# Kernel tuning notes

Measured on AMD Instinct MI355X. Metric: run time of the kernel, lower is better.

## Reference

```python
import jax, jax.numpy as jnp
import numpy as np

NEG_SLOPE = 0.2  # LeakyReLU slope from the module


def setup_inputs() -> dict:
    key = jax.random.key(0)
    k1, k2, k3, k4, k5 = jax.random.split(key, 5)
    B, N, H = 8, 1024, 512
    node_features = jax.random.normal(k1, (B, N, H), dtype=jnp.float32)
    adjacency_matrix = jax.random.randint(k2, (B, N, N), 0, 2, dtype=jnp.int32)
    # attn_linear: Linear(2H, 1). Split weight into src/dst halves (same math as
    # applying it to concat([x_i, x_j])): score_ij = x_i.a_src + x_j.a_dst + b.
    scale = 1.0 / np.sqrt(2 * H)
    attn_w_src = jax.random.uniform(k3, (H,), jnp.float32, -scale, scale)
    attn_w_dst = jax.random.uniform(k4, (H,), jnp.float32, -scale, scale)
    attn_b = jax.random.uniform(k5, (1,), jnp.float32, -scale, scale)
    return {"node_features": node_features, "adjacency_matrix": adjacency_matrix,
            "attn_w_src": attn_w_src, "attn_w_dst": attn_w_dst, "attn_b": attn_b}


def reference(node_features, adjacency_matrix, attn_w_src, attn_w_dst, attn_b):
    B, N, H = node_features.shape
    # Decomposed additive scores: [B,N,1] + [B,1,N] + b  -> [B,N,N]
    s_src = jnp.einsum('bnh,h->bn', node_features, attn_w_src)
    s_dst = jnp.einsum('bnh,h->bn', node_features, attn_w_dst)
    scores = s_src[:, :, None] + s_dst[:, None, :] + attn_b[0]
    scores = jax.nn.leaky_relu(scores, negative_slope=NEG_SLOPE)
    # adjacency + self loops; mask where zero
    adj = adjacency_matrix.astype(jnp.float32) + jnp.eye(N, dtype=jnp.float32)[None]
    scores = jnp.where(adj == 0, -jnp.inf, scores)
    attn = jax.nn.softmax(scores, axis=-1)
    # dropout is identity in eval mode
    return jnp.einsum('bij,bjh->bih', attn, node_features)
```

## Files before the change

### kernel.cpp

```cpp
#include <hip/hip_runtime.h>
#include <hip/hip_bf16.h>

#define BB 8
#define NN 1024
#define HH 512
#define NEG 0.2f

typedef float f32x4 __attribute__((ext_vector_type(4)));
typedef short bf16x8 __attribute__((ext_vector_type(8)));
typedef unsigned int u32;

__device__ __forceinline__ unsigned short f2bf(float f) {
    union { float f; u32 u; } a; a.f = f;
    u32 u = a.u;
    u += 0x7fffu + ((u >> 16) & 1u);
    return (unsigned short)(u >> 16);
}

__device__ __forceinline__ void gload16(const void* g, void* l) {
    __builtin_amdgcn_global_load_lds(
        (const __attribute__((address_space(1))) unsigned int*)g,
        (__attribute__((address_space(3))) unsigned int*)l, 16, 0, 0);
}

__global__ __launch_bounds__(512) void prep_kernel(
    const float* __restrict__ x, const float* __restrict__ wsrc,
    const float* __restrict__ wdst, float* __restrict__ ssrc,
    float* __restrict__ sdst, unsigned short* __restrict__ xt)
{
    __shared__ __align__(16) unsigned short lt[16][528];

    int bid = blockIdx.x;
    int b = bid & 7;
    int j0 = (bid >> 3) * 16;
    int t = threadIdx.x;
    int r = t >> 5;
    int l = t & 31;

    const float* xrow = x + ((size_t)(b * NN + j0 + r)) * HH;
    float psrc = 0.f, pdst = 0.f;
    #pragma unroll
    for (int q = 0; q < 4; ++q) {
        int h = q * 128 + l * 4;
        f32x4 v = *(const f32x4*)(xrow + h);
        f32x4 a = *(const f32x4*)(wsrc + h);
        f32x4 d = *(const f32x4*)(wdst + h);
        psrc += v[0]*a[0] + v[1]*a[1] + v[2]*a[2] + v[3]*a[3];
        pdst += v[0]*d[0] + v[1]*d[1] + v[2]*d[2] + v[3]*d[3];
        u32 lo = (u32)f2bf(v[0]) | ((u32)f2bf(v[1]) << 16);
        u32 hi = (u32)f2bf(v[2]) | ((u32)f2bf(v[3]) << 16);
        *(u32*)&lt[r][h + 0] = lo;
        *(u32*)&lt[r][h + 2] = hi;
    }
    #pragma unroll
    for (int k = 1; k < 32; k <<= 1) {
        psrc += __shfl_xor(psrc, k);
        pdst += __shfl_xor(pdst, k);
    }
    if (l == 0) {
        ssrc[b * NN + j0 + r] = psrc;
        sdst[b * NN + j0 + r] = pdst;
    }
    __syncthreads();

    unsigned short v[16];
    #pragma unroll
    for (int rr = 0; rr < 16; ++rr) v[rr] = lt[rr][t];
    unsigned short* dst = xt + ((size_t)(b * HH + t)) * NN + j0;
    #pragma unroll
    for (int q = 0; q < 2; ++q) {
        bf16x8 pk;
        #pragma unroll
        for (int e = 0; e < 8; ++e) pk[e] = (short)v[q*8 + e];
        *(bf16x8*)(dst + q * 8) = pk;
    }
}

__global__ __launch_bounds__(256) void softmax_kernel(
    const float* __restrict__ ssrc, const float* __restrict__ sdst,
    const int* __restrict__ adj, const float* __restrict__ bptr,
    unsigned short* __restrict__ P)
{
    __shared__ __align__(16) float sd[NN];

    int bid = blockIdx.x;
    int b = bid & 7;
    int r0 = (bid >> 3) * 4;
    int t = threadIdx.x;
    int lane = t & 63;
    int w = t >> 6;

    *(f32x4*)&sd[t * 4] = *(const f32x4*)&sdst[b * NN + t * 4];
    __syncthreads();

    int ig = r0 + w;
    float si = ssrc[b * NN + ig] + bptr[0];
    const int* arow = adj + ((size_t)b * NN + ig) * NN;

    float sc[16];
    float m = -1e30f;
    #pragma unroll
    for (int it = 0; it < 4; ++it) {
        int j = it * 256 + lane * 4;
        int4 a4 = *(const int4*)(arow + j);
        f32x4 sv = *(const f32x4*)&sd[j];
        float s0 = si + sv[0]; s0 = s0 > 0.f ? s0 : NEG * s0;
        float s1 = si + sv[1]; s1 = s1 > 0.f ? s1 : NEG * s1;
        float s2 = si + sv[2]; s2 = s2 > 0.f ? s2 : NEG * s2;
        float s3 = si + sv[3]; s3 = s3 > 0.f ? s3 : NEG * s3;
        sc[it*4+0] = (a4.x != 0 || (j + 0) == ig) ? s0 : -1e30f;
        sc[it*4+1] = (a4.y != 0 || (j + 1) == ig) ? s1 : -1e30f;
        sc[it*4+2] = (a4.z != 0 || (j + 2) == ig) ? s2 : -1e30f;
        sc[it*4+3] = (a4.w != 0 || (j + 3) == ig) ? s3 : -1e30f;
        m = fmaxf(m, fmaxf(fmaxf(sc[it*4+0], sc[it*4+1]), fmaxf(sc[it*4+2], sc[it*4+3])));
    }
    #pragma unroll
    for (int k = 1; k < 64; k <<= 1) m = fmaxf(m, __shfl_xor(m, k));
    float sum = 0.f;
    #pragma unroll
    for (int k = 0; k < 16; ++k) { float e = __expf(sc[k] - m); sc[k] = e; sum += e; }
    #pragma unroll
    for (int k = 1; k < 64; k <<= 1) sum += __shfl_xor(sum, k);
    float inv = 1.f / sum;

    unsigned short* prow = P + ((size_t)b * NN + ig) * NN;
    #pragma unroll
    for (int it = 0; it < 4; ++it) {
        int j = it * 256 + lane * 4;
        u32 lo = (u32)f2bf(sc[it*4+0] * inv) | ((u32)f2bf(sc[it*4+1] * inv) << 16);
        u32 hi = (u32)f2bf(sc[it*4+2] * inv) | ((u32)f2bf(sc[it*4+3] * inv) << 16);
        *(uint2*)(prow + j) = make_uint2(lo, hi);
    }
}

__global__ __launch_bounds__(512) void pv_kernel(
    const unsigned short* __restrict__ P, const unsigned short* __restrict__ xt,
    float* __restrict__ out)
{
    __shared__ __align__(16) unsigned short As[3 * 128 * 64];
    __shared__ __align__(16) unsigned short Bs[3 * 64 * 64];

    int bid = blockIdx.x;
    int b = bid & 7;
    int tt = bid >> 3;
    int h0 = (tt & 3) * 128;
    int i0 = (tt >> 2) * 64;
    int t = threadIdx.x;
    int lane = t & 63;
    int w = t >> 6;
    int wm = w & 3;
    int wn = w >> 2;
    int g = lane >> 4;
    int ln = lane & 15;

    int row0 = t >> 3;
    int c = t & 7;
    int sj = (c ^ (row0 & 7)) * 8;
    const unsigned short* gA0 = xt + ((size_t)(b * HH + h0 + row0)) * NN + sj;
    const unsigned short* gA1 = gA0 + (size_t)64 * NN;
    const unsigned short* gB0 = P + ((size_t)(b * NN + i0 + row0)) * NN + sj;
    unsigned short* lA0 = As + t * 8;
    unsigned short* lA1 = As + 4096 + t * 8;
    unsigned short* lB0 = Bs + t * 8;

    const char* pa[2][2];
    #pragma unroll
    for (int ma = 0; ma < 2; ++ma) {
        int row = wm * 32 + ma * 16 + ln;
        #pragma unroll
        for (int kk = 0; kk < 2; ++kk)
            pa[ma][kk] = (const char*)As + ((row * 128 + kk * 64 + g * 16) ^ ((row & 7) << 4));
    }
    const char* pb[2][2];
    #pragma unroll
    for (int nb = 0; nb < 2; ++nb) {
        int row = wn * 32 + nb * 16 + ln;
        #pragma unroll
        for (int kk = 0; kk < 2; ++kk)
            pb[nb][kk] = (const char*)Bs + ((row * 128 + kk * 64 + g * 16) ^ ((row & 7) << 4));
    }

    f32x4 acc[2][2];
    #pragma unroll
    for (int ma = 0; ma < 2; ++ma)
        #pragma unroll
        for (int nb = 0; nb < 2; ++nb)
            acc[ma][nb] = (f32x4){0.f, 0.f, 0.f, 0.f};

    auto stage = [&](int p, int js) {
        int joff = js * 64;
        gload16(gA0 + joff, lA0 + p * 8192);
        gload16(gA1 + joff, lA1 + p * 8192);
        gload16(gB0 + joff, lB0 + p * 4096);
    };
    auto compute = [&](int ofsA, int ofsB) {
        bf16x8 af[2][2], bfr[2][2];
        #pragma unroll
        for (int ma = 0; ma < 2; ++ma)
            #pragma unroll
            for (int kk = 0; kk < 2; ++kk)
                af[ma][kk] = *(const bf16x8*)(pa[ma][kk] + ofsA);
        #pragma unroll
        for (int nb = 0; nb < 2; ++nb)
            #pragma unroll
            for (int kk = 0; kk < 2; ++kk)
                bfr[nb][kk] = *(const bf16x8*)(pb[nb][kk] + ofsB);
        #pragma unroll
        for (int kk = 0; kk < 2; ++kk)
            #pragma unroll
            for (int ma = 0; ma < 2; ++ma)
                #pragma unroll
                for (int nb = 0; nb < 2; ++nb)
                    acc[ma][nb] = __builtin_amdgcn_mfma_f32_16x16x32_bf16(af[ma][kk], bfr[nb][kk], acc[ma][nb], 0, 0, 0);
    };

    stage(0, 0);
    stage(1, 1);
    int cur = 0, nx2 = 2;
    for (int js = 0; js < 16; ++js) {
        if (js < 15) asm volatile("s_waitcnt vmcnt(3)" ::: "memory");
        else         asm volatile("s_waitcnt vmcnt(0)" ::: "memory");
        __builtin_amdgcn_sched_barrier(0);
        __builtin_amdgcn_s_barrier();
        if (js + 2 < 16) stage(nx2, js + 2);
        compute(cur * 16384, cur * 8192);
        cur = (cur == 2) ? 0 : cur + 1;
        nx2 = (nx2 == 2) ? 0 : nx2 + 1;
    }

    #pragma unroll
    for (int nb = 0; nb < 2; ++nb) {
        int i = i0 + wn * 32 + nb * 16 + ln;
        #pragma unroll
        for (int ma = 0; ma < 2; ++ma) {
            float* dst = out + ((size_t)(b * NN + i)) * HH + h0 + wm * 32 + ma * 16 + g * 4;
            *(f32x4*)dst = acc[ma][nb];
        }
    }
}

extern "C" void kernel_launch(void* const* d_in, const int* in_sizes, int n_in,
                              void* d_out, int out_size, void* d_ws, size_t ws_size,
                              hipStream_t stream) {
    const float* x    = (const float*)d_in[0];
    const int*   adj  = (const int*)d_in[1];
    const float* wsrc = (const float*)d_in[2];
    const float* wdst = (const float*)d_in[3];
    const float* bias = (const float*)d_in[4];
    float* out = (float*)d_out;

    float* ssrc = (float*)d_ws;
    float* sdst = ssrc + BB * NN;
    unsigned short* xt = (unsigned short*)(sdst + BB * NN);
    unsigned short* P  = xt + (size_t)BB * HH * NN;

    prep_kernel<<<dim3(BB * (NN / 16)), dim3(512), 0, stream>>>(x, wsrc, wdst, ssrc, sdst, xt);
    softmax_kernel<<<dim3(BB * NN / 4), dim3(256), 0, stream>>>(ssrc, sdst, adj, bias, P);
    pv_kernel<<<dim3(BB * 4 * 16), dim3(512), 0, stream>>>(P, xt, out);
}
```

Measured before the change: 37.68 us.

## Use 128x128 PV tiles with 32x32 MFMA and split-K across wave groups

The PV GEMM kernel moves from 64x128 to 128x128 output tiles per block, which halves the grid to 256 blocks. It switches to 32x32x16 bf16 MFMA instructions and splits the K loop between two wave groups that handle alternating stages. The partial sums are then reduced through LDS. This is meant to improve operand reuse and reduce redundant global loads of xt. In exchange it lowers parallelism to 256 blocks, about one per CU, and adds a reduction pass.

Result: no change. 37.18 us (-1.3%).

```diff
diff --git a/kernel.cpp b/kernel.cpp
--- a/kernel.cpp
+++ b/kernel.cpp
@@ -7,6 +7,7 @@
 #define NEG 0.2f
 
 typedef float f32x4 __attribute__((ext_vector_type(4)));
+typedef float f32x16 __attribute__((ext_vector_type(16)));
 typedef short bf16x8 __attribute__((ext_vector_type(8)));
 typedef unsigned int u32;
 
@@ -137,21 +138,24 @@
     const unsigned short* __restrict__ P, const unsigned short* __restrict__ xt,
     float* __restrict__ out)
 {
-    __shared__ __align__(16) unsigned short As[3 * 128 * 64];
-    __shared__ __align__(16) unsigned short Bs[3 * 64 * 64];
+    __shared__ __align__(16) unsigned short LDSq[3 * 8192 * 2];
+    unsigned short* As = LDSq;
+    unsigned short* Bs = LDSq + 3 * 8192;
 
     int bid = blockIdx.x;
     int b = bid & 7;
     int tt = bid >> 3;
     int h0 = (tt & 3) * 128;
-    int i0 = (tt >> 2) * 64;
+    int i0 = (tt >> 2) * 128;
     int t = threadIdx.x;
     int lane = t & 63;
     int w = t >> 6;
-    int wm = w & 3;
-    int wn = w >> 2;
-    int g = lane >> 4;
-    int ln = lane & 15;
+    int ks = w >> 2;
+    int wsub = w & 3;
+    int wm = wsub & 1;
+    int wn = wsub >> 1;
+    int r32 = lane & 31;
+    int hi = lane >> 5;
 
     int row0 = t >> 3;
     int c = t & 7;
@@ -159,82 +163,105 @@
     const unsigned short* gA0 = xt + ((size_t)(b * HH + h0 + row0)) * NN + sj;
     const unsigned short* gA1 = gA0 + (size_t)64 * NN;
     const unsigned short* gB0 = P + ((size_t)(b * NN + i0 + row0)) * NN + sj;
+    const unsigned short* gB1 = gB0 + (size_t)64 * NN;
     unsigned short* lA0 = As + t * 8;
     unsigned short* lA1 = As + 4096 + t * 8;
     unsigned short* lB0 = Bs + t * 8;
-
-    const char* pa[2][2];
+    unsigned short* lB1 = Bs + 4096 + t * 8;
+
+    const char* Ab[2]; int aswz[2];
     #pragma unroll
     for (int ma = 0; ma < 2; ++ma) {
-        int row = wm * 32 + ma * 16 + ln;
-        #pragma unroll
-        for (int kk = 0; kk < 2; ++kk)
-            pa[ma][kk] = (const char*)As + ((row * 128 + kk * 64 + g * 16) ^ ((row & 7) << 4));
-    }
-    const char* pb[2][2];
+        int row = wm * 64 + ma * 32 + r32;
+        Ab[ma] = (const char*)As + row * 128;
+        aswz[ma] = (row & 7) << 4;
+    }
+    const char* Bb[2]; int bswz[2];
     #pragma unroll
     for (int nb = 0; nb < 2; ++nb) {
-        int row = wn * 32 + nb * 16 + ln;
-        #pragma unroll
-        for (int kk = 0; kk < 2; ++kk)
-            pb[nb][kk] = (const char*)Bs + ((row * 128 + kk * 64 + g * 16) ^ ((row & 7) << 4));
-    }
-
-    f32x4 acc[2][2];
-    #pragma unroll
-    for (int ma = 0; ma < 2; ++ma)
-        #pragma unroll
-        for (int nb = 0; nb < 2; ++nb)
-            acc[ma][nb] = (f32x4){0.f, 0.f, 0.f, 0.f};
+        int row = wn * 64 + nb * 32 + r32;
+        Bb[nb] = (const char*)Bs + row * 128;
+        bswz[nb] = (row & 7) << 4;
+    }
+
+    f32x16 acc00 = {}, acc01 = {}, acc10 = {}, acc11 = {};
 
     auto stage = [&](int p, int js) {
         int joff = js * 64;
         gload16(gA0 + joff, lA0 + p * 8192);
         gload16(gA1 + joff, lA1 + p * 8192);
-        gload16(gB0 + joff, lB0 + p * 4096);
+        gload16(gB0 + joff, lB0 + p * 8192);
+        gload16(gB1 + joff, lB1 + p * 8192);
     };
-    auto compute = [&](int ofsA, int ofsB) {
-        bf16x8 af[2][2], bfr[2][2];
-        #pragma unroll
-        for (int ma = 0; ma < 2; ++ma)
-            #pragma unroll
-            for (int kk = 0; kk < 2; ++kk)
-                af[ma][kk] = *(const bf16x8*)(pa[ma][kk] + ofsA);
-        #pragma unroll
-        for (int nb = 0; nb < 2; ++nb)
-            #pragma unroll
-            for (int kk = 0; kk < 2; ++kk)
-                bfr[nb][kk] = *(const bf16x8*)(pb[nb][kk] + ofsB);
-        #pragma unroll
-        for (int kk = 0; kk < 2; ++kk)
-            #pragma unroll
-            for (int ma = 0; ma < 2; ++ma)
-                #pragma unroll
-                for (int nb = 0; nb < 2; ++nb)
-                    acc[ma][nb] = __builtin_amdgcn_mfma_f32_16x16x32_bf16(af[ma][kk], bfr[nb][kk], acc[ma][nb], 0, 0, 0);
+    auto compute = [&](int p) {
+        int ofs = p * 16384;
+        #pragma unroll
+        for (int cc = 0; cc < 4; ++cc) {
+            int koff = cc * 32 + hi * 16;
+            bf16x8 af0 = *(const bf16x8*)(Ab[0] + (koff ^ aswz[0]) + ofs);
+            bf16x8 af1 = *(const bf16x8*)(Ab[1] + (koff ^ aswz[1]) + ofs);
+            bf16x8 bf0 = *(const bf16x8*)(Bb[0] + (koff ^ bswz[0]) + ofs);
+            bf16x8 bf1 = *(const bf16x8*)(Bb[1] + (koff ^ bswz[1]) + ofs);
+            acc00 = __builtin_amdgcn_mfma_f32_32x32x16_bf16(af0, bf0, acc00, 0, 0, 0);
+            acc01 = __builtin_amdgcn_mfma_f32_32x32x16_bf16(af0, bf1, acc01, 0, 0, 0);
+            acc10 = __builtin_amdgcn_mfma_f32_32x32x16_bf16(af1, bf0, acc10, 0, 0, 0);
+            acc11 = __builtin_amdgcn_mfma_f32_32x32x16_bf16(af1, bf1, acc11, 0, 0, 0);
+        }
     };
 
     stage(0, 0);
     stage(1, 1);
-    int cur = 0, nx2 = 2;
+    #pragma unroll
     for (int js = 0; js < 16; ++js) {
-        if (js < 15) asm volatile("s_waitcnt vmcnt(3)" ::: "memory");
+        if (js < 15) asm volatile("s_waitcnt vmcnt(4)" ::: "memory");
         else         asm volatile("s_waitcnt vmcnt(0)" ::: "memory");
         __builtin_amdgcn_sched_barrier(0);
         __builtin_amdgcn_s_barrier();
-        if (js + 2 < 16) stage(nx2, js + 2);
-        compute(cur * 16384, cur * 8192);
-        cur = (cur == 2) ? 0 : cur + 1;
-        nx2 = (nx2 == 2) ? 0 : nx2 + 1;
-    }
-
-    #pragma unroll
-    for (int nb = 0; nb < 2; ++nb) {
-        int i = i0 + wn * 32 + nb * 16 + ln;
+        __builtin_amdgcn_sched_barrier(0);
+        if (js + 2 < 16) stage((js + 2) % 3, js + 2);
+        if ((js & 1) == ks) compute(js % 3);
+    }
+
+    __syncthreads();
+
+    float* red = (float*)LDSq;
+    int ridx = (wsub * 64 + lane) * 68;
+    if (ks == 1) {
+        #pragma unroll
+        for (int fq = 0; fq < 4; ++fq) {
+            const f32x16* a = fq == 0 ? &acc00 : fq == 1 ? &acc01 : fq == 2 ? &acc10 : &acc11;
+            #pragma unroll
+            for (int q = 0; q < 4; ++q)
+                *(f32x4*)(red + ridx + fq * 16 + q * 4) =
+                    (f32x4){(*a)[q*4+0], (*a)[q*4+1], (*a)[q*4+2], (*a)[q*4+3]};
+        }
+    }
+    __syncthreads();
+    if (ks == 0) {
+        #pragma unroll
+        for (int fq = 0; fq < 4; ++fq) {
+            f32x16* a = fq == 0 ? &acc00 : fq == 1 ? &acc01 : fq == 2 ? &acc10 : &acc11;
+            #pragma unroll
+            for (int q = 0; q < 4; ++q) {
+                f32x4 v = *(const f32x4*)(red + ridx + fq * 16 + q * 4);
+                (*a)[q*4+0] += v[0]; (*a)[q*4+1] += v[1];
+                (*a)[q*4+2] += v[2]; (*a)[q*4+3] += v[3];
+            }
+        }
         #pragma unroll
         for (int ma = 0; ma < 2; ++ma) {
-            float* dst = out + ((size_t)(b * NN + i)) * HH + h0 + wm * 32 + ma * 16 + g * 4;
-            *(f32x4*)dst = acc[ma][nb];
+            #pragma unroll
+            for (int nb = 0; nb < 2; ++nb) {
+                const f32x16* a = ma == 0 ? (nb == 0 ? &acc00 : &acc01)
+                                          : (nb == 0 ? &acc10 : &acc11);
+                int i = i0 + wn * 64 + nb * 32 + r32;
+                float* drow = out + ((size_t)(b * NN + i)) * HH + h0 + wm * 64 + ma * 32;
+                #pragma unroll
+                for (int q = 0; q < 4; ++q) {
+                    f32x4 v = {(*a)[q*4+0], (*a)[q*4+1], (*a)[q*4+2], (*a)[q*4+3]};
+                    *(f32x4*)(drow + q * 8 + hi * 4) = v;
+                }
+            }
         }
     }
 }
@@ -256,5 +283,5 @@
 
     prep_kernel<<<dim3(BB * (NN / 16)), dim3(512), 0, stream>>>(x, wsrc, wdst, ssrc, sdst, xt);
     softmax_kernel<<<dim3(BB * NN / 4), dim3(256), 0, stream>>>(ssrc, sdst, adj, bias, P);
-    pv_kernel<<<dim3(BB * 4 * 16), dim3(512), 0, stream>>>(P, xt, out);
-}
+    pv_kernel<<<dim3(BB * 4 * 8), dim3(512), 0, stream>>>(P, xt, out);
+}
```
